# Kernel tuning notes

Hardware: AMD Instinct MI355X
Metric: run time of the kernel (lower is better)

The kernel has to match this reference:

```python
import jax, jax.numpy as jnp
import numpy as np
from jax import lax

B, NMEAS, M, LAYER_NUM = 2048, 128, 256, 10
CLAMP_MIN, CLAMP_MAX = 1e-6, 100.0
EPS_S = 1e-6


def _conv2d(x, w, b):
    y = lax.conv_general_dilated(x, w, (1, 1), 'SAME', dimension_numbers=('NCHW', 'OIHW', 'NCHW'))
    return y + b[None, :, None, None]


def _conv1d(x, w, b):
    y = lax.conv_general_dilated(x, w, (1,), 'SAME', dimension_numbers=('NCH', 'OIH', 'NCH'))
    return y + b[None, :, None]


def setup_inputs():
    key = jax.random.key(0)
    ks = jax.random.split(key, 12)
    s = 1.0 / np.sqrt(2.0 * NMEAS)  # ~unit-norm dictionary columns
    return {
        'Yr': jax.random.normal(ks[0], (B, 1, NMEAS, 1), jnp.float32),
        'Yi': jax.random.normal(ks[1], (B, 1, NMEAS, 1), jnp.float32),
        'Ar': s * jax.random.normal(ks[2], (NMEAS, M), jnp.float32),
        'Ai': s * jax.random.normal(ks[3], (NMEAS, M), jnp.float32),
        'conv1_w': 0.1 * jax.random.normal(ks[4], (32, 2, 3, 3), jnp.float32),
        'conv1_b': jnp.zeros((32,), jnp.float32),
        'conv2_w': 0.1 * jax.random.normal(ks[5], (64, 32, 3, 3), jnp.float32),
        'conv2_b': jnp.zeros((64,), jnp.float32),
        'hc_w': 0.1 * jax.random.normal(ks[6], (LAYER_NUM - 1, 64, 3), jnp.float32),
        'hc_b': jnp.zeros((LAYER_NUM - 1,), jnp.float32),
        'hd_w': 0.1 * jax.random.normal(ks[7], (LAYER_NUM - 1, 64, 3), jnp.float32),
        'hd_b': jnp.zeros((LAYER_NUM - 1,), jnp.float32),
        'hT_w': 0.1 * jax.random.normal(ks[8], (LAYER_NUM, 64, 3), jnp.float32),
        'hT_b': jnp.zeros((LAYER_NUM,), jnp.float32),
        'a0': jnp.asarray(1.0, jnp.float32),
        'b0': jnp.asarray(1.0, jnp.float32),
    }


def _hypernet(ay, c1w, c1b, c2w, c2b, hcw, hcb, hdw, hdb, hTw, hTb):
    # ay: [B, 2, M]; batch acts as image width (context)
    x_img = jnp.transpose(ay, (1, 2, 0))[None]              # [1, 2, M, B]
    f = jax.nn.relu(_conv2d(x_img, c1w, c1b))               # [1, 32, M, B]
    f = jax.nn.relu(_conv2d(f, c2w, c2b))                   # [1, 64, M, B]
    f = jnp.mean(f, axis=2)                                 # AdaptiveAvgPool2d((1,None)) -> [1, 64, B]
    c = jnp.abs(_conv1d(f, hcw, hcb))[0].T                  # [B, L-1]
    d = jnp.abs(_conv1d(f, hdw, hdb))[0].T                  # [B, L-1]
    T = jnp.abs(_conv1d(f, hTw, hTb))[0].T                  # [B, L]
    c = jnp.clip(c, CLAMP_MIN, CLAMP_MAX)
    d = jnp.maximum(d, CLAMP_MIN)
    T = jnp.clip(T, CLAMP_MIN, CLAMP_MAX)
    return c, d, T


def _forward(Yr, Yi, Ar, Ai, conv1_w, conv1_b, conv2_w, conv2_b,
             hc_w, hc_b, hd_w, hd_b, hT_w, hT_b, a0, b0):
    Y = (Yr + 1j * Yi).astype(jnp.complex64)                # [B,1,Nmeas,1]
    A = (Ar + 1j * Ai).astype(jnp.complex64)                # [Nmeas,M]
    AT = A.conj().T                                         # [M,Nmeas]
    AA = AT @ A                                             # [M,M] Hermitian
    AY = jnp.matmul(AT, Y)                                  # [B,1,M,1]
    b = Y.shape[0]
    n = Y.shape[2]
    ay = jnp.concatenate([AY.real.reshape(b, 1, -1), AY.imag.reshape(b, 1, -1)], axis=1)  # [B,2,M]
    c, d, T = _hypernet(ay, conv1_w, conv1_b, conv2_w, conv2_b,
                        hc_w, hc_b, hd_w, hd_b, hT_w, hT_b)
    D = jnp.real(jnp.diagonal(AA))[None, None, :, None]     # diag of Hermitian AA is real; [1,1,M,1]
    eps = (a0 / b0).astype(jnp.complex64) * jnp.ones((b, 1, 1, 1), jnp.complex64)
    Lam = ((c[:, 0] / d[:, 0])[:, None, None, None] * jnp.ones((1, 1, M, 1), jnp.float32)).astype(jnp.complex64)
    U = jnp.zeros((b, 1, M, 1), jnp.complex64)
    a = a0 + n
    for k in range(LAYER_NUM - 1):
        Tk = T[:, k][:, None, None, None]
        # fused SBL/VAMP mean update
        U = eps * (Tk * U - jnp.matmul(AA, U) + AY) / (eps * Tk + Lam + EPS_S)
        Sigma = 1.0 / (eps * D + Lam + EPS_S)
        r = Y - jnp.matmul(A, U)
        eps1 = jnp.sum(r.real ** 2 + r.imag ** 2, axis=(2, 3), keepdims=True)  # ||.||_F^2
        eps2 = jnp.sum(D * Sigma, axis=(2, 3), keepdims=True)
        eps = a / (b0 + eps1 + eps2 + EPS_S)
        Lam = (c[:, k][:, None, None, None] + 1.0) / (
            d[:, k][:, None, None, None] + jnp.abs(U) ** 2 + Sigma + EPS_S)
    Tk = T[:, LAYER_NUM - 1][:, None, None, None]
    U = eps * (Tk * U - jnp.matmul(AA, U) + AY) / (eps * Tk + Lam + EPS_S)
    Ua = jnp.abs(U)
    Ua = Ua / (jnp.max(Ua) + 1e-8)
    return Ua, c, d, T


def reference(Yr, Yi, Ar, Ai, conv1_w, conv1_b, conv2_w, conv2_b,
              hc_w, hc_b, hd_w, hd_b, hT_w, hT_b, a0, b0):
    Ua, c, d, T = _forward(Yr, Yi, Ar, Ai, conv1_w, conv1_b, conv2_w, conv2_b,
                           hc_w, hc_b, hd_w, hd_b, hT_w, hT_b, a0, b0)
    # original returns the last batch row of c/d/T (detached diagnostics)
    return Ua, c[-1:, :], d[-1:, :], T[-1:, :]
```

## Files before the change

### kernel.cpp

```cpp
#include <hip/hip_runtime.h>
#include <math.h>

#define B_N   2048
#define NM    128
#define M_N   256
#define LNUM  10
#define EPS_Sf 1e-6f

typedef _Float16 half8 __attribute__((ext_vector_type(8)));
typedef float floatx4 __attribute__((ext_vector_type(4)));

__device__ __forceinline__ float frcp(float x) { return __builtin_amdgcn_rcpf(x); }

static constexpr size_t o_AA  = 0;
static constexpr size_t o_D   = o_AA  + 131072;
static constexpr size_t o_yn  = o_D   + 256;
static constexpr size_t o_AY  = o_yn  + 2048;
static constexpr size_t o_AYt = o_AY  + 1048576;
static constexpr size_t o_w2t = o_AYt + 1048576;
static constexpr size_t o_z1  = o_w2t + 18432;
static constexpr size_t o_fp  = o_z1  + 16777216;
static constexpr size_t o_f   = o_fp  + 2097152;
static constexpr size_t o_c   = o_f   + 131072;
static constexpr size_t o_dd  = o_c   + 18432;
static constexpr size_t o_T   = o_dd  + 18432;
static constexpr size_t o_Ua  = o_T   + 20480;
static constexpr size_t o_gm  = o_Ua  + 524288;

__global__ void k_pre(const float* __restrict__ Ar, const float* __restrict__ Ai,
                      const float* __restrict__ Yr, const float* __restrict__ Yi,
                      const float* __restrict__ w2, float* __restrict__ ws) {
    __shared__ float sb[2048];
    int blk = blockIdx.x;
    int tid = threadIdx.x;
    if (blk < 256) {
        float* cr = sb; float* ci = sb + NM;
        int i = blk, j = tid;
        if (j < NM) { cr[j] = Ar[j * M_N + i]; ci[j] = Ai[j * M_N + i]; }
        __syncthreads();
        float sr = 0.f, si = 0.f;
        for (int n = 0; n < NM; ++n) {
            float ar = Ar[n * M_N + j], ai = Ai[n * M_N + j];
            sr += cr[n] * ar + ci[n] * ai;
            si += cr[n] * ai - ci[n] * ar;
        }
        _Float16* A16 = (_Float16*)(ws + o_AA);
        size_t off = ((size_t)((i >> 4) * 8 + (j >> 5)) * 64
                      + (size_t)(((j >> 3) & 3) * 16 + (i & 15))) * 8 + (j & 7);
        A16[off]         = (_Float16)sr;
        A16[65536 + off] = (_Float16)si;
        if (j == i) ws[o_D + i] = sr;
        if (i == 0 && j == 0) *(unsigned int*)(ws + o_gm) = 0u;
    } else if (blk < 328) {
        int i = (blk - 256) * 256 + tid;
        if (i < 64 * 32 * 9) {
            int oc = i / 288, r = i % 288;
            int ic = r / 9, kk = r % 9;
            _Float16* Wa = (_Float16*)(ws + o_w2t);
            Wa[((size_t)oc * 9 + kk) * 32 + ic] = (_Float16)w2[i];
        }
    } else if (blk < 584) {
        float2* Ys = (float2*)sb;
        int bb0 = (blk - 328) * 8;
        for (int i = tid; i < 8 * NM; i += 256) {
            int g = i >> 7, n = i & 127;
            Ys[g * NM + n] = make_float2(Yr[(size_t)(bb0 + g) * NM + n],
                                         Yi[(size_t)(bb0 + g) * NM + n]);
        }
        __syncthreads();
        if (tid < 8) {
            float s = 0.f;
            for (int n = 0; n < NM; ++n) { float2 y = Ys[tid * NM + n]; s += y.x * y.x + y.y * y.y; }
            ws[o_yn + bb0 + tid] = s;
        }
        int m = tid;
        float accr[8], acci[8];
#pragma unroll
        for (int g = 0; g < 8; ++g) { accr[g] = 0.f; acci[g] = 0.f; }
        for (int n = 0; n < NM; ++n) {
            float ar = Ar[n * M_N + m], ai = Ai[n * M_N + m];
#pragma unroll
            for (int g = 0; g < 8; ++g) {
                float2 y = Ys[g * NM + n];
                accr[g] += ar * y.x + ai * y.y;
                acci[g] += ar * y.y - ai * y.x;
            }
        }
        float2* AY = (float2*)(ws + o_AY);
#pragma unroll
        for (int g = 0; g < 8; ++g) {
            AY[(size_t)(bb0 + g) * M_N + m] = make_float2(accr[g], acci[g]);
            ws[o_AYt + (size_t)m * B_N + (bb0 + g)] = accr[g];
            ws[o_AYt + 524288 + (size_t)m * B_N + (bb0 + g)] = acci[g];
        }
    } else {
        size_t idx = (size_t)(blk - 584) * 1024 + (size_t)tid * 4;
        *(float4*)(ws + o_f + idx) = make_float4(0.f, 0.f, 0.f, 0.f);
    }
}

#define MFMA16(A,Bv,C) C = __builtin_amdgcn_mfma_f32_16x16x32_f16(A, Bv, C, 0, 0, 0)
__global__ void __launch_bounds__(256)
k_conv12(const float* __restrict__ w1, const float* __restrict__ b1,
         const float* __restrict__ b2, float* __restrict__ ws) {
    __shared__ __align__(16) _Float16 zt[324 * 44];
    __shared__ __align__(16) _Float16 xsf[800];
    int tid = threadIdx.x;
    int lane = tid & 63, w = tid >> 6;
    int col = lane & 15, quad = lane >> 4;
    int bt = blockIdx.x & 127, g = blockIdx.x >> 7;
    int b0 = bt * 16, m0 = g * 16;

    const _Float16* Wa = (const _Float16*)(ws + o_w2t);
    int oc0w = w * 16;
    half8 Af[9];
#pragma unroll
    for (int kk = 0; kk < 9; ++kk)
        Af[kk] = *(const half8*)(Wa + ((size_t)(oc0w + col) * 9 + kk) * 32 + quad * 8);
    float bias2[4];
#pragma unroll
    for (int r = 0; r < 4; ++r) bias2[r] = b2[oc0w + quad * 4 + r];

    half8 Aw[2];
#pragma unroll
    for (int t = 0; t < 2; ++t)
#pragma unroll
        for (int j = 0; j < 8; ++j) {
            int k = quad * 8 + j;
            int oc = t * 16 + col;
            Aw[t][j] = (k < 18) ? (_Float16)w1[oc * 18 + (k & 1) * 9 + (k >> 1)]
                                : (_Float16)0.f;
        }
    float b1a[4], b1b[4];
#pragma unroll
    for (int r = 0; r < 4; ++r) { b1a[r] = b1[quad * 4 + r]; b1b[r] = b1[16 + quad * 4 + r]; }

    int basej[8];
#pragma unroll
    for (int j = 0; j < 8; ++j) {
        int k = quad * 8 + j;
        int c = k & 1, e = k >> 1;
        int dm = (e * 11) >> 5;
        int db = e - dm * 3;
        basej[j] = (k < 18) ? (c * 400 + dm * 20 + db) : 0;
    }

    const float* xr = ws + o_AYt;
    for (int i = tid; i < 800; i += 256) {
        int c = (i >= 400) ? 1 : 0;
        int rem = i - c * 400;
        int r = (rem * 205) >> 12;
        int q = rem - r * 20;
        int row = m0 - 2 + r, bc = b0 - 2 + q;
        float v = (((unsigned)row < (unsigned)M_N) && ((unsigned)bc < (unsigned)B_N))
                    ? xr[(size_t)c * 524288 + (size_t)row * B_N + bc] : 0.f;
        xsf[i] = (_Float16)v;
    }
    __syncthreads();

    for (int grp = w; grp < 21; grp += 4) {
        int p = grp * 16 + col;
        bool pok = (p < 324);
        int mz = (p * 57) >> 10;
        int bz = p - mz * 18;
        if (!pok) { mz = 0; bz = 0; }
        int base = mz * 20 + bz;
        half8 xb;
#pragma unroll
        for (int j = 0; j < 8; ++j) xb[j] = xsf[basej[j] + base];
        floatx4 z0 = (floatx4){0.f, 0.f, 0.f, 0.f};
        floatx4 z1v = (floatx4){0.f, 0.f, 0.f, 0.f};
        MFMA16(Aw[0], xb, z0);
        MFMA16(Aw[1], xb, z1v);
        bool zok = ((unsigned)(m0 - 1 + mz) < (unsigned)M_N) &&
                   ((unsigned)(b0 - 1 + bz) < (unsigned)B_N);
        unsigned long long u0 = 0ull, u1 = 0ull;
        if (zok) {
            union { _Float16 h[4]; unsigned long long u; } a;
#pragma unroll
            for (int r = 0; r < 4; ++r) a.h[r] = (_Float16)fmaxf(z0[r] + b1a[r], 0.f);
            u0 = a.u;
#pragma unroll
            for (int r = 0; r < 4; ++r) a.h[r] = (_Float16)fmaxf(z1v[r] + b1b[r], 0.f);
            u1 = a.u;
        }
        if (pok) {
            _Float16* d = zt + (size_t)p * 44 + quad * 4;
            *(unsigned long long*)(d)      = u0;
            *(unsigned long long*)(d + 16) = u1;
        }
    }
    __syncthreads();

    const _Float16* zb = zt + (size_t)col * 44 + (size_t)quad * 8;
    half8 Bf[3][3];
#pragma unroll
    for (int ph = 0; ph < 3; ++ph)
#pragma unroll
        for (int db = 0; db < 3; ++db)
            Bf[ph][db] = *(const half8*)(zb + (size_t)ph * 792 + (size_t)db * 44);

    floatx4 facc = (floatx4){0.f, 0.f, 0.f, 0.f};
#pragma unroll
    for (int mm = 0; mm < 16; ++mm) {
        floatx4 a0 = (floatx4){0.f, 0.f, 0.f, 0.f};
#pragma unroll
        for (int dm = 0; dm < 3; ++dm) {
            int ph = (mm + dm) % 3;
#pragma unroll
            for (int db = 0; db < 3; ++db)
                MFMA16(Af[dm * 3 + db], Bf[ph][db], a0);
        }
#pragma unroll
        for (int r = 0; r < 4; ++r) facc[r] += fmaxf(a0[r] + bias2[r], 0.f);
        if (mm < 15) {
            int ph = mm % 3;
#pragma unroll
            for (int db = 0; db < 3; ++db)
                Bf[ph][db] = *(const half8*)(zb + (size_t)(mm + 3) * 792 + (size_t)db * 44);
        }
    }
    float* f = ws + o_f;
#pragma unroll
    for (int r = 0; r < 4; ++r)
        atomicAdd(&f[(size_t)(oc0w + quad * 4 + r) * B_N + b0 + col], facc[r]);
}

__global__ void k_cdt(const float* __restrict__ hcw, const float* __restrict__ hcb,
                      const float* __restrict__ hdw, const float* __restrict__ hdb,
                      const float* __restrict__ hTw, const float* __restrict__ hTb,
                      float* __restrict__ ws, float* __restrict__ out) {
    int l = blockIdx.x >> 3;
    int b = (blockIdx.x & 7) * 256 + threadIdx.x;
    const float* f = ws + o_f;
    const float* w; float bi; int li, kind;
    if (l < 9)       { kind = 0; li = l;      w = hcw + (size_t)li * 192; bi = hcb[li]; }
    else if (l < 18) { kind = 1; li = l - 9;  w = hdw + (size_t)li * 192; bi = hdb[li]; }
    else             { kind = 2; li = l - 18; w = hTw + (size_t)li * 192; bi = hTb[li]; }
    __shared__ float wsm[192];
    for (int i = threadIdx.x; i < 192; i += 256) wsm[i] = w[i] * (1.f / 256.f);
    __syncthreads();
    float acc = bi;
    bool okL = (b > 0), okR = (b < B_N - 1);
    for (int ic = 0; ic < 64; ++ic) {
        const float* fr = f + (size_t)ic * B_N + b;
        float fm1 = okL ? fr[-1] : 0.f;
        float f0  = fr[0];
        float fp1 = okR ? fr[1] : 0.f;
        acc += fm1 * wsm[ic * 3] + f0 * wsm[ic * 3 + 1] + fp1 * wsm[ic * 3 + 2];
    }
    float v = fmaxf(fabsf(acc), 1e-6f);
    if (kind != 1) v = fminf(v, 100.f);
    if (kind == 0)      { ws[o_c  + (size_t)b * 9  + li] = v; if (b == B_N - 1) out[524288 + li] = v; }
    else if (kind == 1) { ws[o_dd + (size_t)b * 9  + li] = v; if (b == B_N - 1) out[524297 + li] = v; }
    else                { ws[o_T  + (size_t)b * 10 + li] = v; if (b == B_N - 1) out[524306 + li] = v; }
}

__global__ void __launch_bounds__(512, 2)
k_iter(const float* __restrict__ a0p, const float* __restrict__ b0p, float* __restrict__ ws) {
    __shared__ __align__(16) _Float16 Ubf[2][8][64][8];
    __shared__ __align__(16) float redv[16][28];
    __shared__ float redm[8];
    int tid = threadIdx.x;
    int lane = tid & 63, w = tid >> 6;
    int col = lane & 15, quad = lane >> 4;
    int b = blockIdx.x * 16 + col;

    for (int i = tid; i < 16 * 28; i += 512) ((float*)redv)[i] = 0.f;

    const float2* AY = (const float2*)(ws + o_AY);
    const _Float16* Af = (const _Float16*)(ws + o_AA);
    float a0 = a0p[0], b0v = b0p[0];
    float atot = a0 + (float)NM;
    float yn = ws[o_yn + b];
    float eps = a0 / b0v;

    half8 Ar8[2][8], Ai8[2][8];
#pragma unroll
    for (int t = 0; t < 2; ++t)
#pragma unroll
        for (int ks = 0; ks < 8; ++ks) {
            const _Float16* ab = Af + (((size_t)(w * 2 + t) * 8 + ks) * 64 + lane) * 8;
            Ar8[t][ks] = *(const half8*)(ab);
            Ai8[t][ks] = *(const half8*)(ab + 65536);
        }

    float Dv[8], ayr[8], ayi[8], lam[8], Ur[8], Ui[8];
    float c0h = ws[o_c + (size_t)b * 9];
    float d0h = ws[o_dd + (size_t)b * 9];
    float T0 = ws[o_T + (size_t)b * 10];
    float lam0 = c0h * frcp(d0h);
#pragma unroll
    for (int ri = 0; ri < 8; ++ri) {
        int m = w * 32 + (ri >> 2) * 16 + quad * 4 + (ri & 3);
        Dv[ri] = ws[o_D + m];
        float2 a = AY[(size_t)b * M_N + m];
        ayr[ri] = a.x; ayi[ri] = a.y;
        lam[ri] = lam0;
    }
    {
        float iv = eps * frcp(fmaf(eps, T0, lam0 + EPS_Sf));
#pragma unroll
        for (int ri = 0; ri < 8; ++ri) { Ur[ri] = iv * ayr[ri]; Ui[ri] = iv * ayi[ri]; }
    }

    int laneD0 = ((quad >> 1)) * 16 + col;
    int laneD1 = (2 + (quad >> 1)) * 16 + col;
    int eb = (quad & 1) * 4;

    for (int k = 0; k < LNUM - 1; ++k) {
        float ck = ws[o_c + (size_t)b * 9 + k];
        float dk = ws[o_dd + (size_t)b * 9 + k];
        float Tn = ws[o_T + (size_t)b * 10 + k + 1];
        {
            union { _Float16 h[4]; unsigned long long u; } pk;
#pragma unroll
            for (int t = 0; t < 2; ++t) {
                int ld = t ? laneD1 : laneD0;
#pragma unroll
                for (int r = 0; r < 4; ++r) pk.h[r] = (_Float16)Ur[t * 4 + r];
                *(unsigned long long*)&Ubf[0][w][ld][eb] = pk.u;
#pragma unroll
                for (int r = 0; r < 4; ++r) pk.h[r] = (_Float16)Ui[t * 4 + r];
                *(unsigned long long*)&Ubf[1][w][ld][eb] = pk.u;
            }
        }
        __syncthreads();
        floatx4 ac[8];
#pragma unroll
        for (int i = 0; i < 8; ++i) ac[i] = (floatx4){0.f, 0.f, 0.f, 0.f};
#pragma unroll
        for (int ks = 0; ks < 8; ++ks) {
            half8 urh = *(const half8*)&Ubf[0][ks][lane][0];
            half8 uih = *(const half8*)&Ubf[1][ks][lane][0];
            MFMA16(Ar8[0][ks], urh, ac[0]);
            MFMA16(Ai8[0][ks], uih, ac[1]);
            MFMA16(Ar8[0][ks], uih, ac[2]);
            MFMA16(Ai8[0][ks], urh, ac[3]);
            MFMA16(Ar8[1][ks], urh, ac[4]);
            MFMA16(Ai8[1][ks], uih, ac[5]);
            MFMA16(Ar8[1][ks], uih, ac[6]);
            MFMA16(Ai8[1][ks], urh, ac[7]);
        }
        float wr[8], wi[8], sg[8];
        float p1 = 0.f, p2 = 0.f, p3 = 0.f;
#pragma unroll
        for (int t = 0; t < 2; ++t)
#pragma unroll
            for (int r = 0; r < 4; ++r) {
                int ri = t * 4 + r;
                wr[ri] = ac[t * 4 + 0][r] - ac[t * 4 + 1][r];
                wi[ri] = ac[t * 4 + 2][r] + ac[t * 4 + 3][r];
                sg[ri] = frcp(fmaf(eps, Dv[ri], lam[ri] + EPS_Sf));
                p1 += ayr[ri] * Ur[ri] + ayi[ri] * Ui[ri];
                p2 += Ur[ri] * wr[ri] + Ui[ri] * wi[ri];
                p3 += Dv[ri] * sg[ri];
            }
        p1 += __shfl_xor(p1, 16); p1 += __shfl_xor(p1, 32);
        p2 += __shfl_xor(p2, 16); p2 += __shfl_xor(p2, 32);
        p3 += __shfl_xor(p3, 16); p3 += __shfl_xor(p3, 32);
        if (lane < 16) {
            redv[col][w * 3]     = p1;
            redv[col][w * 3 + 1] = p2;
            redv[col][w * 3 + 2] = p3;
        }
        __syncthreads();
        float s[3] = {0.f, 0.f, 0.f};
#pragma unroll
        for (int j = 0; j < 7; ++j) {
            floatx4 v4 = *(const floatx4*)&redv[col][j * 4];
#pragma unroll
            for (int e = 0; e < 4; ++e) s[(j * 4 + e) % 3] += v4[e];
        }
        float eps1 = fmaxf(yn - 2.f * s[0] + s[1], 0.f);
        eps = atot * frcp(b0v + eps1 + s[2] + EPS_Sf);
        float ck1 = ck + 1.f;
#pragma unroll
        for (int ri = 0; ri < 8; ++ri) {
            lam[ri] = ck1 * frcp(dk + Ur[ri] * Ur[ri] + Ui[ri] * Ui[ri] + sg[ri] + EPS_Sf);
            float iv = eps * frcp(fmaf(eps, Tn, lam[ri] + EPS_Sf));
            Ur[ri] = iv * (Tn * Ur[ri] - wr[ri] + ayr[ri]);
            Ui[ri] = iv * (Tn * Ui[ri] - wi[ri] + ayi[ri]);
        }
    }
    float lm = 0.f;
#pragma unroll
    for (int t = 0; t < 2; ++t) {
        float4 v;
        v.x = sqrtf(Ur[t * 4 + 0] * Ur[t * 4 + 0] + Ui[t * 4 + 0] * Ui[t * 4 + 0]);
        v.y = sqrtf(Ur[t * 4 + 1] * Ur[t * 4 + 1] + Ui[t * 4 + 1] * Ui[t * 4 + 1]);
        v.z = sqrtf(Ur[t * 4 + 2] * Ur[t * 4 + 2] + Ui[t * 4 + 2] * Ui[t * 4 + 2]);
        v.w = sqrtf(Ur[t * 4 + 3] * Ur[t * 4 + 3] + Ui[t * 4 + 3] * Ui[t * 4 + 3]);
        *(float4*)&ws[o_Ua + (size_t)b * M_N + w * 32 + t * 16 + quad * 4] = v;
        lm = fmaxf(lm, fmaxf(fmaxf(v.x, v.y), fmaxf(v.z, v.w)));
    }
#pragma unroll
    for (int off = 32; off >= 1; off >>= 1) lm = fmaxf(lm, __shfl_xor(lm, off));
    if (lane == 0) redm[w] = lm;
    __syncthreads();
    if (tid == 0) {
        float mx = redm[0];
#pragma unroll
        for (int i = 1; i < 8; ++i) mx = fmaxf(mx, redm[i]);
        atomicMax((unsigned int*)(ws + o_gm), __float_as_uint(mx));
    }
}

__global__ void k_norm(const float* __restrict__ ws, float* __restrict__ out) {
    size_t i = (size_t)blockIdx.x * 256 + threadIdx.x;
    float gm = __uint_as_float(*(const unsigned int*)(ws + o_gm));
    out[i] = ws[o_Ua + i] / (gm + 1e-8f);
}

extern "C" void kernel_launch(void* const* d_in, const int* in_sizes, int n_in,
                              void* d_out, int out_size, void* d_ws, size_t ws_size,
                              hipStream_t stream) {
    (void)in_sizes; (void)n_in; (void)out_size; (void)ws_size;
    const float* Yr  = (const float*)d_in[0];
    const float* Yi  = (const float*)d_in[1];
    const float* Ar  = (const float*)d_in[2];
    const float* Ai  = (const float*)d_in[3];
    const float* w1  = (const float*)d_in[4];
    const float* b1  = (const float*)d_in[5];
    const float* w2  = (const float*)d_in[6];
    const float* b2  = (const float*)d_in[7];
    const float* hcw = (const float*)d_in[8];
    const float* hcb = (const float*)d_in[9];
    const float* hdw = (const float*)d_in[10];
    const float* hdb = (const float*)d_in[11];
    const float* hTw = (const float*)d_in[12];
    const float* hTb = (const float*)d_in[13];
    const float* a0  = (const float*)d_in[14];
    const float* b0  = (const float*)d_in[15];
    float* ws = (float*)d_ws;
    float* out = (float*)d_out;

    k_pre   <<<712, 256, 0, stream>>>(Ar, Ai, Yr, Yi, w2, ws);
    k_conv12<<<2048, 256, 0, stream>>>(w1, b1, b2, ws);
    k_cdt   <<<224, 256, 0, stream>>>(hcw, hcb, hdw, hdb, hTw, hTb, ws, out);
    k_iter  <<<128, 512, 0, stream>>>(a0, b0, ws);
    k_norm  <<<2048, 256, 0, stream>>>(ws, out);
}
```

Baseline: 233.5 us.

## Split conv2 row loop across two wave halves and break MFMA dependency chain

k_conv12 now launches 512 threads per block. The second group of four waves handles rows 8-15 of the 16-row tile while the first handles rows 0-7, and their partial pooled sums are reduced through shared memory before the atomic add. Each row's nine MFMAs are also spread across three independent accumulators instead of one serial chain, which shortens the MFMA dependency latency. The cost is an extra LDS reduction, two more barriers, doubled per-thread weight fragment loads across the block, and possibly lower occupancy from register pressure.

```diff
diff --git a/kernel.cpp b/kernel.cpp
--- a/kernel.cpp
+++ b/kernel.cpp
@@ -100,7 +100,7 @@
 }
 
 #define MFMA16(A,Bv,C) C = __builtin_amdgcn_mfma_f32_16x16x32_f16(A, Bv, C, 0, 0, 0)
-__global__ void __launch_bounds__(256)
+__global__ void __launch_bounds__(512)
 k_conv12(const float* __restrict__ w1, const float* __restrict__ b1,
          const float* __restrict__ b2, float* __restrict__ ws) {
     __shared__ __align__(16) _Float16 zt[324 * 44];
@@ -108,11 +108,13 @@
     int tid = threadIdx.x;
     int lane = tid & 63, w = tid >> 6;
     int col = lane & 15, quad = lane >> 4;
+    int wo = w & 3;
+    int mh = w >> 2;
     int bt = blockIdx.x & 127, g = blockIdx.x >> 7;
     int b0 = bt * 16, m0 = g * 16;
 
     const _Float16* Wa = (const _Float16*)(ws + o_w2t);
-    int oc0w = w * 16;
+    int oc0w = wo * 16;
     half8 Af[9];
 #pragma unroll
     for (int kk = 0; kk < 9; ++kk)
@@ -146,7 +148,7 @@
     }
 
     const float* xr = ws + o_AYt;
-    for (int i = tid; i < 800; i += 256) {
+    for (int i = tid; i < 800; i += 512) {
         int c = (i >= 400) ? 1 : 0;
         int rem = i - c * 400;
         int r = (rem * 205) >> 12;
@@ -158,7 +160,7 @@
     }
     __syncthreads();
 
-    for (int grp = w; grp < 21; grp += 4) {
+    for (int grp = w; grp < 21; grp += 8) {
         int p = grp * 16 + col;
         bool pok = (p < 324);
         int mz = (p * 57) >> 10;
@@ -198,32 +200,44 @@
     for (int ph = 0; ph < 3; ++ph)
 #pragma unroll
         for (int db = 0; db < 3; ++db)
-            Bf[ph][db] = *(const half8*)(zb + (size_t)ph * 792 + (size_t)db * 44);
+            Bf[(mh * 8 + ph) % 3][db] =
+                *(const half8*)(zb + (size_t)(mh * 8 + ph) * 792 + (size_t)db * 44);
 
     floatx4 facc = (floatx4){0.f, 0.f, 0.f, 0.f};
 #pragma unroll
-    for (int mm = 0; mm < 16; ++mm) {
+    for (int ml = 0; ml < 8; ++ml) {
+        int mz = mh * 8 + ml;
         floatx4 a0 = (floatx4){0.f, 0.f, 0.f, 0.f};
-#pragma unroll
-        for (int dm = 0; dm < 3; ++dm) {
-            int ph = (mm + dm) % 3;
+        floatx4 a1 = (floatx4){0.f, 0.f, 0.f, 0.f};
+        floatx4 a2 = (floatx4){0.f, 0.f, 0.f, 0.f};
+#pragma unroll
+        for (int db = 0; db < 3; ++db) {
+            MFMA16(Af[0 * 3 + db], Bf[(mz + 0) % 3][db], a0);
+            MFMA16(Af[1 * 3 + db], Bf[(mz + 1) % 3][db], a1);
+            MFMA16(Af[2 * 3 + db], Bf[(mz + 2) % 3][db], a2);
+        }
+#pragma unroll
+        for (int r = 0; r < 4; ++r)
+            facc[r] += fmaxf(a0[r] + a1[r] + a2[r] + bias2[r], 0.f);
+        if (ml < 7) {
+            int ph = mz % 3;
 #pragma unroll
             for (int db = 0; db < 3; ++db)
-                MFMA16(Af[dm * 3 + db], Bf[ph][db], a0);
-        }
-#pragma unroll
-        for (int r = 0; r < 4; ++r) facc[r] += fmaxf(a0[r] + bias2[r], 0.f);
-        if (mm < 15) {
-            int ph = mm % 3;
-#pragma unroll
-            for (int db = 0; db < 3; ++db)
-                Bf[ph][db] = *(const half8*)(zb + (size_t)(mm + 3) * 792 + (size_t)db * 44);
-        }
-    }
-    float* f = ws + o_f;
-#pragma unroll
-    for (int r = 0; r < 4; ++r)
-        atomicAdd(&f[(size_t)(oc0w + quad * 4 + r) * B_N + b0 + col], facc[r]);
+                Bf[ph][db] = *(const half8*)(zb + (size_t)(mz + 3) * 792 + (size_t)db * 44);
+        }
+    }
+    __syncthreads();
+    float* redf = (float*)zt;
+    if (mh == 1)
+        *(floatx4*)&redf[((size_t)wo * 64 + lane) * 4] = facc;
+    __syncthreads();
+    if (mh == 0) {
+        floatx4 o = *(const floatx4*)&redf[((size_t)wo * 64 + lane) * 4];
+        float* f = ws + o_f;
+#pragma unroll
+        for (int r = 0; r < 4; ++r)
+            atomicAdd(&f[(size_t)(oc0w + quad * 4 + r) * B_N + b0 + col], facc[r] + o[r]);
+    }
 }
 
 __global__ void k_cdt(const float* __restrict__ hcw, const float* __restrict__ hcb,
@@ -436,7 +450,7 @@
     float* out = (float*)d_out;
 
     k_pre   <<<712, 256, 0, stream>>>(Ar, Ai, Yr, Yi, w2, ws);
-    k_conv12<<<2048, 256, 0, stream>>>(w1, b1, b2, ws);
+    k_conv12<<<2048, 512, 0, stream>>>(w1, b1, b2, ws);
     k_cdt   <<<224, 256, 0, stream>>>(hcw, hcb, hdw, hdb, hTw, hTb, ws, out);
     k_iter  <<<128, 512, 0, stream>>>(a0, b0, ws);
     k_norm  <<<2048, 256, 0, stream>>>(ws, out);
```

New measurement: 382.5 us. 63.8% more time.
